# Kernel tuning notes

Measured on AMD Instinct MI355X. Metric: run time of the kernel, lower is better.

The kernel has to match this reference:

```python
import jax, jax.numpy as jnp
import numpy as np

B, L, E = 4, 2048, 1024
H, DQ, DV = 8, 128, 128
SCALE = 1.0 / np.sqrt(DQ).astype(np.float32)


def setup_inputs() -> dict:
    key = jax.random.key(0)
    ks = jax.random.split(key, 6)
    return {
        "qInputs": jax.random.normal(ks[0], (B, L, E), dtype=jnp.float32),
        "kvInputs": jax.random.normal(ks[1], (B, L, E), dtype=jnp.float32),
        "mask": jnp.zeros((B, H, L, L), dtype=jnp.bool_),
        "W_Q": jax.random.normal(ks[2], (E, H * DQ), dtype=jnp.float32) * 0.02,
        "W_K": jax.random.normal(ks[3], (E, H * DQ), dtype=jnp.float32) * 0.02,
        "W_V": jax.random.normal(ks[4], (E, H * DV), dtype=jnp.float32) * 0.02,
        "W_fc": jax.random.normal(ks[5], (H * DV, E), dtype=jnp.float32) * 0.02,
    }


def reference(qInputs, kvInputs, mask, W_Q, W_K, W_V, W_fc):
    b, lq, _ = qInputs.shape
    lk = kvInputs.shape[1]
    # Projections -> [B, H, L, D]
    Q = (qInputs @ W_Q).reshape(b, lq, H, DQ).transpose(0, 2, 1, 3)
    K = (kvInputs @ W_K).reshape(b, lk, H, DQ).transpose(0, 2, 1, 3)
    V = (kvInputs @ W_V).reshape(b, lk, H, DV).transpose(0, 2, 1, 3)
    # Scaled dot-product with additive mask fill of -1e9
    scores = jnp.einsum("bhqd,bhkd->bhqk", Q, K) * SCALE
    scores = jnp.where(mask, jnp.float32(-1e9), scores)
    attn = jax.nn.softmax(scores, axis=-1)
    ctx = jnp.einsum("bhqk,bhkd->bhqd", attn, V)
    ctx = ctx.transpose(0, 2, 1, 3).reshape(b, lq, H * DV)
    return ctx @ W_fc
```

## Files before the change

kernel.cpp:

```cpp
#include <hip/hip_runtime.h>
#include <stdint.h>

#define LQ 2048
#define EDIM 1024
#define HN 8
#define DH 128
#define BATCH 4
#define SCALE_LOG2E 0.12753785051263942f

typedef short bf16x8 __attribute__((ext_vector_type(8)));
typedef float f32x4 __attribute__((ext_vector_type(4)));
typedef unsigned short u16;
typedef unsigned short u16x4 __attribute__((ext_vector_type(4)));

__device__ __forceinline__ u16 f2bf(float f) {
  union { float f; uint32_t u; } c; c.f = f;
  uint32_t u = c.u;
  return (u16)((u + 0x7fffu + ((u >> 16) & 1u)) >> 16);
}

__device__ __forceinline__ void async16(const void* g, void* l) {
  __builtin_amdgcn_global_load_lds((const __attribute__((address_space(1))) void*)g,
                                   (__attribute__((address_space(3))) void*)l, 16, 0, 0);
}

__device__ __forceinline__ uint32_t lds_b(const u16* p) {
  return (uint32_t)(uintptr_t)(__attribute__((address_space(3))) const u16*)p;
}
__device__ __forceinline__ void ldsr4_issue(bf16x8& d0, bf16x8& d1, bf16x8& d2, bf16x8& d3,
                                            uint32_t a0, uint32_t a1, uint32_t a2, uint32_t a3) {
  asm volatile("ds_read_b128 %0, %4\n\t"
               "ds_read_b128 %1, %5\n\t"
               "ds_read_b128 %2, %6\n\t"
               "ds_read_b128 %3, %7"
               : "=&v"(d0), "=&v"(d1), "=&v"(d2), "=&v"(d3)
               : "v"(a0), "v"(a1), "v"(a2), "v"(a3));
}
template <int N>
__device__ __forceinline__ void lgkm_wait_sb() {
  asm volatile("s_waitcnt lgkmcnt(%0)" :: "n"(N) : "memory");
  __builtin_amdgcn_sched_barrier(0);
}
__device__ __forceinline__ uint32_t cvtpk(float lo, float hi) {
  uint32_t r;
  asm("v_cvt_pk_bf16_f32 %0, %1, %2" : "=v"(r) : "v"(lo), "v"(hi));
  return r;
}
__device__ __forceinline__ void plane_swap(uint32_t& a, uint32_t& b) {
#if __has_builtin(__builtin_amdgcn_permlane32_swap) && __has_builtin(__builtin_amdgcn_permlane16_swap)
  auto r1 = __builtin_amdgcn_permlane32_swap(a, b, false, false);
  auto r2 = __builtin_amdgcn_permlane16_swap(r1[0], r1[1], false, false);
  a = r2[0];
  b = r2[1];
#else
  asm("s_nop 1\n\t"
      "v_permlane32_swap_b32 %0, %1\n\t"
      "s_nop 1\n\t"
      "v_permlane16_swap_b32 %0, %1\n\t"
      "s_nop 1"
      : "+v"(a), "+v"(b));
#endif
}
__device__ __forceinline__ float xorsum16(float x) {
#if __has_builtin(__builtin_amdgcn_permlane16_swap)
  union { float f; uint32_t u; } c; c.f = x;
  auto r = __builtin_amdgcn_permlane16_swap(c.u, c.u, false, false);
  union { uint32_t u; float f; } a, b; a.u = r[0]; b.u = r[1];
  return a.f + b.f;
#else
  return x + __shfl_xor(x, 16);
#endif
}
__device__ __forceinline__ float xorsum32(float x) {
#if __has_builtin(__builtin_amdgcn_permlane32_swap)
  union { float f; uint32_t u; } c; c.f = x;
  auto r = __builtin_amdgcn_permlane32_swap(c.u, c.u, false, false);
  union { uint32_t u; float f; } a, b; a.u = r[0]; b.u = r[1];
  return a.f + b.f;
#else
  return x + __shfl_xor(x, 32);
#endif
}
__device__ __forceinline__ void swz64(int& x, int& y) {
  const int f = x + 64 * y;
  x = (f & 7) * 8 + ((f >> 3) & 7);
  y = f >> 6;
}

__global__ __launch_bounds__(256) void prep_kernel(const float* __restrict__ qIn, const float* __restrict__ kvIn,
                                                   const float* __restrict__ w0, const float* __restrict__ w1,
                                                   const float* __restrict__ w2, const float* __restrict__ w3,
                                                   u16* __restrict__ oq, u16* __restrict__ okv,
                                                   u16* __restrict__ o0, u16* __restrict__ o1,
                                                   u16* __restrict__ o2, u16* __restrict__ o3) {
  __shared__ float tile[32][33];
  const int bid = blockIdx.x;
  const int t = threadIdx.x;
  if (bid < 16384) {
    const float* in = (bid >= 8192) ? kvIn : qIn;
    u16* out = (bid >= 8192) ? okv : oq;
    size_t i = (size_t)(bid & 8191) * 256 + t;
    float4 v = ((const float4*)in)[i];
    u16x4 o;
    o.x = f2bf(v.x); o.y = f2bf(v.y); o.z = f2bf(v.z); o.w = f2bf(v.w);
    ((u16x4*)out)[i] = o;
  } else {
    const int idx = bid - 16384;
    const int z = idx >> 10;
    const int rem = idx & 1023;
    const float* in; u16* out;
    switch (z) {
      case 0: in = w0; out = o0; break;
      case 1: in = w1; out = o1; break;
      case 2: in = w2; out = o2; break;
      default: in = w3; out = o3; break;
    }
    const int tx = t & 31, ty = t >> 5;
    const int x0 = (rem & 31) * 32;
    const int y0 = (rem >> 5) * 32;
#pragma unroll
    for (int j = 0; j < 32; j += 8)
      tile[ty + j][tx] = in[(size_t)(y0 + ty + j) * EDIM + x0 + tx];
    __syncthreads();
#pragma unroll
    for (int j = 0; j < 32; j += 8)
      out[(size_t)(x0 + ty + j) * EDIM + (y0 + tx)] = f2bf(tile[tx][ty + j]);
  }
}

struct GemmCore {
  template <typename EpiF>
  static __device__ __forceinline__ void run(const u16* __restrict__ A, const u16* __restrict__ Bt,
                                             int m0, int n0, u16* As, u16* Bs, EpiF epi) {
    const int tid = threadIdx.x;
    const int l = tid & 63;
    const int w = tid >> 6;
    const int wm = (w >> 1) * 64;
    const int wn = (w & 1) * 64;
    const int fm = l & 15;
    const int q4 = l >> 4;
    const int f7 = fm & 7;
    f32x4 acc[4][4] = {};
    for (int k0 = 0; k0 < EDIM; k0 += 64) {
      __syncthreads();
#pragma unroll
      for (int ii = 0; ii < 4; ++ii) {
        const int rloc = w * 32 + ii * 8 + (l >> 3);
        const int cs = (l & 7) ^ (rloc & 7);
        async16(A + (size_t)(m0 + rloc) * EDIM + k0 + cs * 8, &As[(w * 32 + ii * 8) * 64 + l * 8]);
        async16(Bt + (size_t)(n0 + rloc) * EDIM + k0 + cs * 8, &Bs[(w * 32 + ii * 8) * 64 + l * 8]);
      }
      __syncthreads();
#pragma unroll
      for (int ks = 0; ks < 2; ++ks) {
        const int coff = ((ks * 4 + q4) ^ f7) * 8;
        bf16x8 a[4], b[4];
#pragma unroll
        for (int i = 0; i < 4; ++i) a[i] = *(const bf16x8*)&As[(wm + i * 16 + fm) * 64 + coff];
#pragma unroll
        for (int j = 0; j < 4; ++j) b[j] = *(const bf16x8*)&Bs[(wn + j * 16 + fm) * 64 + coff];
#pragma unroll
        for (int i = 0; i < 4; ++i)
#pragma unroll
          for (int j = 0; j < 4; ++j)
            acc[i][j] = __builtin_amdgcn_mfma_f32_16x16x32_bf16(a[i], b[j], acc[i][j], 0, 0, 0);
      }
    }
    const int rr = q4 * 4;
#pragma unroll
    for (int i = 0; i < 4; ++i)
#pragma unroll
      for (int j = 0; j < 4; ++j)
#pragma unroll
        for (int r = 0; r < 4; ++r)
          epi(m0 + wm + i * 16 + rr + r, n0 + wn + j * 16 + fm, acc[i][j][r]);
  }
};

__global__ __launch_bounds__(256) void qkv_gemm(const u16* __restrict__ xq, const u16* __restrict__ xkv,
                                                const u16* __restrict__ WqT, const u16* __restrict__ WkT,
                                                const u16* __restrict__ WvT,
                                                u16* __restrict__ Qb, u16* __restrict__ Kb,
                                                u16* __restrict__ Vt) {
  __shared__ __align__(16) u16 As[128 * 64];
  __shared__ __align__(16) u16 Bs[128 * 64];
  const int z = blockIdx.z;
  int bx = blockIdx.x, by = blockIdx.y;
  swz64(bx, by);
  if (z == 0) {
    GemmCore::run(xq, WqT, bx * 128, by * 128, As, Bs,
                  [&](int gm, int gn, float v) { Qb[(size_t)gm * EDIM + gn] = f2bf(v * SCALE_LOG2E); });
  } else if (z == 1) {
    GemmCore::run(xkv, WkT, bx * 128, by * 128, As, Bs,
                  [&](int gm, int gn, float v) { Kb[(size_t)gm * EDIM + gn] = f2bf(v); });
  } else {
    GemmCore::run(WvT, xkv, by * 128, bx * 128, As, Bs,
                  [&](int gm, int gn, float v) {
                    Vt[((size_t)(gn >> 11) * 1024 + gm) * 2048 + (gn & 2047)] = f2bf(v);
                  });
  }
}

__global__ __launch_bounds__(256) void out_gemm(const u16* __restrict__ ctx, const u16* __restrict__ WfcT,
                                                float* __restrict__ out) {
  __shared__ __align__(16) u16 As[128 * 64];
  __shared__ __align__(16) u16 Bs[128 * 64];
  int bx = blockIdx.x, by = blockIdx.y;
  swz64(bx, by);
  GemmCore::run(ctx, WfcT, bx * 128, by * 128, As, Bs,
                [&](int gm, int gn, float v) { out[(size_t)gm * EDIM + gn] = v; });
}

__global__ __launch_bounds__(256, 2) void attn_kernel(const u16* __restrict__ Qb, const u16* __restrict__ Kb,
                                                      const u16* __restrict__ Vt,
                                                      const unsigned char* __restrict__ mask,
                                                      u16* __restrict__ ctx) {
  __shared__ __align__(16) u16 Ktile[2][64 * 128];
  __shared__ __align__(16) u16 Vtile[2][128 * 64];
  const int tid = threadIdx.x;
  const int l = tid & 63;
  const int w = tid >> 6;
  const int flat = blockIdx.x;
  const int xcd = flat & 7;
  const int idx = flat >> 3;
  const int panel = xcd * 4 + (idx >> 4);
  const int qt = idx & 15;
  const int h = panel & 7;
  const int b = panel >> 3;
  const int fm = l & 15;
  const int q4 = l >> 4;
  const int fk = q4 * 8;
  const int f7 = fm & 7;
  const int qbase = qt * 128 + w * 32;
  const int bh = b * HN + h;

  const u16* Kbh = Kb + (size_t)b * LQ * EDIM + h * DH;
  const u16* Vth = Vt + (size_t)bh * DH * LQ;
  const size_t mbase = (size_t)bh * (size_t)LQ * LQ;
  const unsigned char* mscan = mask + mbase + (size_t)(qbase + (l >> 1)) * LQ + (l & 1) * 64;

  bf16x8 qf[2][4];
#pragma unroll
  for (int mt = 0; mt < 2; ++mt)
#pragma unroll
    for (int ks = 0; ks < 4; ++ks)
      qf[mt][ks] = *(const bf16x8*)(Qb + (size_t)(b * LQ + qbase + mt * 16 + fm) * EDIM + h * DH + ks * 32 + fk);

  uint32_t curAcc = 0, nxtAcc = 0;
#pragma unroll
  for (int j = 0; j < 4; ++j) {
    uint4 mv = *(const uint4*)(mscan + j * 16);
    curAcc |= mv.x | mv.y | mv.z | mv.w;
  }

  auto stageK = [&](int kt_, int buf) {
#pragma unroll
    for (int ii = 0; ii < 4; ++ii) {
      const int i = w * 4 + ii;
      const int row = i * 4 + (l >> 4);
      const int g = (l & 15) ^ (row & 7);
      async16(Kbh + (size_t)(kt_ * 64 + row) * EDIM + g * 8, &Ktile[buf][i * 512 + l * 8]);
    }
  };
  auto stageV = [&](int kt_, int buf) {
#pragma unroll
    for (int ii = 0; ii < 4; ++ii) {
      const int i = w * 4 + ii;
      const int row = i * 8 + (l >> 3);
      const int g = (l & 7) ^ (row & 7);
      async16(Vth + (size_t)row * LQ + kt_ * 64 + g * 8, &Vtile[buf][i * 512 + l * 8]);
    }
  };

  stageK(0, 0);
  stageV(0, 0);

  f32x4 o[2][8] = {};
  float lsumv[2] = {0.f, 0.f};

  for (int it = 0; it < 32; ++it) {
    const int cur = it & 1;
    __syncthreads();
    if (it + 1 < 32) { stageK(it + 1, 1 - cur); stageV(it + 1, 1 - cur); }

    if ((it & 1) == 0) {
      if (it > 0) curAcc = nxtAcc;
      nxtAcc = 0;
      const int tn = (it >> 1) + 1;
      if (tn < 16) {
        const unsigned char* ms = mscan + tn * 128;
#pragma unroll
        for (int j = 0; j < 4; ++j) {
          uint4 mv = *(const uint4*)(ms + j * 16);
          nxtAcc |= mv.x | mv.y | mv.z | mv.w;
        }
      }
    }
    const int hasMask = __any(curAcc != 0);

    const u16* KT = &Ktile[cur][0];
    const u16* VT = &Vtile[cur][0];

    f32x4 st[4][2] = {};
    bf16x8 kf[2][4];
    bf16x8 v0, v1, v2, v3, v4, v5, v6, v7;
    bf16x8 x0, x1, x2, x3, x4, x5, x6, x7;
    {
      const int slot = q4 ^ f7;
      ldsr4_issue(kf[0][0], kf[0][1], kf[0][2], kf[0][3],
                  lds_b(KT + (0 * 16 + fm) * 128 + slot * 8),
                  lds_b(KT + (1 * 16 + fm) * 128 + slot * 8),
                  lds_b(KT + (2 * 16 + fm) * 128 + slot * 8),
                  lds_b(KT + (3 * 16 + fm) * 128 + slot * 8));
    }
#pragma unroll
    for (int ks = 0; ks < 3; ++ks) {
      const int c = ks & 1;
      const int slot = ((ks + 1) * 4 + q4) ^ f7;
      ldsr4_issue(kf[c ^ 1][0], kf[c ^ 1][1], kf[c ^ 1][2], kf[c ^ 1][3],
                  lds_b(KT + (0 * 16 + fm) * 128 + slot * 8),
                  lds_b(KT + (1 * 16 + fm) * 128 + slot * 8),
                  lds_b(KT + (2 * 16 + fm) * 128 + slot * 8),
                  lds_b(KT + (3 * 16 + fm) * 128 + slot * 8));
      lgkm_wait_sb<4>();
      __builtin_amdgcn_s_setprio(1);
#pragma unroll
      for (int mt = 0; mt < 2; ++mt) {
        st[0][mt] = __builtin_amdgcn_mfma_f32_16x16x32_bf16(kf[c][0], qf[mt][ks], st[0][mt], 0, 0, 0);
        st[1][mt] = __builtin_amdgcn_mfma_f32_16x16x32_bf16(kf[c][1], qf[mt][ks], st[1][mt], 0, 0, 0);
        st[2][mt] = __builtin_amdgcn_mfma_f32_16x16x32_bf16(kf[c][2], qf[mt][ks], st[2][mt], 0, 0, 0);
        st[3][mt] = __builtin_amdgcn_mfma_f32_16x16x32_bf16(kf[c][3], qf[mt][ks], st[3][mt], 0, 0, 0);
      }
      __builtin_amdgcn_s_setprio(0);
    }
    {
      const int vs0 = q4 ^ f7;
      ldsr4_issue(v0, v1, v2, v3,
                  lds_b(VT + (0 * 16 + fm) * 64 + vs0 * 8), lds_b(VT + (1 * 16 + fm) * 64 + vs0 * 8),
                  lds_b(VT + (2 * 16 + fm) * 64 + vs0 * 8), lds_b(VT + (3 * 16 + fm) * 64 + vs0 * 8));
      ldsr4_issue(v4, v5, v6, v7,
                  lds_b(VT + (4 * 16 + fm) * 64 + vs0 * 8), lds_b(VT + (5 * 16 + fm) * 64 + vs0 * 8),
                  lds_b(VT + (6 * 16 + fm) * 64 + vs0 * 8), lds_b(VT + (7 * 16 + fm) * 64 + vs0 * 8));
      lgkm_wait_sb<8>();
      __builtin_amdgcn_s_setprio(1);
#pragma unroll
      for (int mt = 0; mt < 2; ++mt) {
        st[0][mt] = __builtin_amdgcn_mfma_f32_16x16x32_bf16(kf[1][0], qf[mt][3], st[0][mt], 0, 0, 0);
        st[1][mt] = __builtin_amdgcn_mfma_f32_16x16x32_bf16(kf[1][1], qf[mt][3], st[1][mt], 0, 0, 0);
        st[2][mt] = __builtin_amdgcn_mfma_f32_16x16x32_bf16(kf[1][2], qf[mt][3], st[2][mt], 0, 0, 0);
        st[3][mt] = __builtin_amdgcn_mfma_f32_16x16x32_bf16(kf[1][3], qf[mt][3], st[3][mt], 0, 0, 0);
      }
      __builtin_amdgcn_s_setprio(0);
    }

    uint32_t pk[2][4][2];
    float sA[2], sB[2];
    bf16x8 paf0, paf1;
#pragma unroll
    for (int mt = 0; mt < 2; ++mt) {
      float sum = 0.f;
      if (hasMask) {
        const unsigned char* mrow = mask + mbase + (size_t)(qbase + mt * 16 + fm) * LQ + it * 64 + q4 * 4;
#pragma unroll
        for (int kt = 0; kt < 2; ++kt) {
          const uint32_t mv = *(const uint32_t*)(mrow + kt * 16);
#pragma unroll
          for (int r = 0; r < 4; ++r) {
            float e = ((mv >> (8 * r)) & 0xffu) ? 0.f : exp2f(st[kt][mt][r]);
            st[kt][mt][r] = e;
            sum += e;
          }
        }
      } else {
#pragma unroll
        for (int kt = 0; kt < 2; ++kt)
#pragma unroll
          for (int r = 0; r < 4; ++r) {
            float e = exp2f(st[kt][mt][r]);
            st[kt][mt][r] = e;
            sum += e;
          }
      }
      sA[mt] = sum;
      pk[mt][0][0] = cvtpk(st[0][mt][0], st[0][mt][1]);
      pk[mt][0][1] = cvtpk(st[0][mt][2], st[0][mt][3]);
      pk[mt][1][0] = cvtpk(st[1][mt][0], st[1][mt][1]);
      pk[mt][1][1] = cvtpk(st[1][mt][2], st[1][mt][3]);
    }
    {
      union { uint32_t u[4]; bf16x8 v; } fb;
      uint32_t e0 = pk[0][0][0], f0 = pk[0][1][0];
      uint32_t e1 = pk[0][0][1], f1 = pk[0][1][1];
      plane_swap(e0, f0); plane_swap(e1, f1);
      fb.u[0] = e0; fb.u[1] = e1; fb.u[2] = f0; fb.u[3] = f1;
      paf0 = fb.v;
      uint32_t g0 = pk[1][0][0], h0 = pk[1][1][0];
      uint32_t g1 = pk[1][0][1], h1 = pk[1][1][1];
      plane_swap(g0, h0); plane_swap(g1, h1);
      fb.u[0] = g0; fb.u[1] = g1; fb.u[2] = h0; fb.u[3] = h1;
      paf1 = fb.v;
    }
    {
      const int vs1 = (4 + q4) ^ f7;
      ldsr4_issue(x0, x1, x2, x3,
                  lds_b(VT + (0 * 16 + fm) * 64 + vs1 * 8), lds_b(VT + (1 * 16 + fm) * 64 + vs1 * 8),
                  lds_b(VT + (2 * 16 + fm) * 64 + vs1 * 8), lds_b(VT + (3 * 16 + fm) * 64 + vs1 * 8));
      ldsr4_issue(x4, x5, x6, x7,
                  lds_b(VT + (4 * 16 + fm) * 64 + vs1 * 8), lds_b(VT + (5 * 16 + fm) * 64 + vs1 * 8),
                  lds_b(VT + (6 * 16 + fm) * 64 + vs1 * 8), lds_b(VT + (7 * 16 + fm) * 64 + vs1 * 8));
    }
    lgkm_wait_sb<8>();
    __builtin_amdgcn_s_setprio(1);
    o[0][0] = __builtin_amdgcn_mfma_f32_16x16x32_bf16(paf0, v0, o[0][0], 0, 0, 0);
    o[1][0] = __builtin_amdgcn_mfma_f32_16x16x32_bf16(paf1, v0, o[1][0], 0, 0, 0);
    o[0][1] = __builtin_amdgcn_mfma_f32_16x16x32_bf16(paf0, v1, o[0][1], 0, 0, 0);
    o[1][1] = __builtin_amdgcn_mfma_f32_16x16x32_bf16(paf1, v1, o[1][1], 0, 0, 0);
    o[0][2] = __builtin_amdgcn_mfma_f32_16x16x32_bf16(paf0, v2, o[0][2], 0, 0, 0);
    o[1][2] = __builtin_amdgcn_mfma_f32_16x16x32_bf16(paf1, v2, o[1][2], 0, 0, 0);
    o[0][3] = __builtin_amdgcn_mfma_f32_16x16x32_bf16(paf0, v3, o[0][3], 0, 0, 0);
    o[1][3] = __builtin_amdgcn_mfma_f32_16x16x32_bf16(paf1, v3, o[1][3], 0, 0, 0);
    o[0][4] = __builtin_amdgcn_mfma_f32_16x16x32_bf16(paf0, v4, o[0][4], 0, 0, 0);
    o[1][4] = __builtin_amdgcn_mfma_f32_16x16x32_bf16(paf1, v4, o[1][4], 0, 0, 0);
    o[0][5] = __builtin_amdgcn_mfma_f32_16x16x32_bf16(paf0, v5, o[0][5], 0, 0, 0);
    o[1][5] = __builtin_amdgcn_mfma_f32_16x16x32_bf16(paf1, v5, o[1][5], 0, 0, 0);
    o[0][6] = __builtin_amdgcn_mfma_f32_16x16x32_bf16(paf0, v6, o[0][6], 0, 0, 0);
    o[1][6] = __builtin_amdgcn_mfma_f32_16x16x32_bf16(paf1, v6, o[1][6], 0, 0, 0);
    o[0][7] = __builtin_amdgcn_mfma_f32_16x16x32_bf16(paf0, v7, o[0][7], 0, 0, 0);
    o[1][7] = __builtin_amdgcn_mfma_f32_16x16x32_bf16(paf1, v7, o[1][7], 0, 0, 0);
    __builtin_amdgcn_s_setprio(0);

#pragma unroll
    for (int mt = 0; mt < 2; ++mt) {
      float sum = 0.f;
      if (hasMask) {
        const unsigned char* mrow = mask + mbase + (size_t)(qbase + mt * 16 + fm) * LQ + it * 64 + q4 * 4;
#pragma unroll
        for (int kt = 2; kt < 4; ++kt) {
          const uint32_t mv = *(const uint32_t*)(mrow + kt * 16);
#pragma unroll
          for (int r = 0; r < 4; ++r) {
            float e = ((mv >> (8 * r)) & 0xffu) ? 0.f : exp2f(st[kt][mt][r]);
            st[kt][mt][r] = e;
            sum += e;
          }
        }
      } else {
#pragma unroll
        for (int kt = 2; kt < 4; ++kt)
#pragma unroll
          for (int r = 0; r < 4; ++r) {
            float e = exp2f(st[kt][mt][r]);
            st[kt][mt][r] = e;
            sum += e;
          }
      }
      sB[mt] = sum;
      pk[mt][2][0] = cvtpk(st[2][mt][0], st[2][mt][1]);
      pk[mt][2][1] = cvtpk(st[2][mt][2], st[2][mt][3]);
      pk[mt][3][0] = cvtpk(st[3][mt][0], st[3][mt][1]);
      pk[mt][3][1] = cvtpk(st[3][mt][2], st[3][mt][3]);
    }
    {
      union { uint32_t u[4]; bf16x8 v; } fb;
      uint32_t e0 = pk[0][2][0], f0 = pk[0][3][0];
      uint32_t e1 = pk[0][2][1], f1 = pk[0][3][1];
      plane_swap(e0, f0); plane_swap(e1, f1);
      fb.u[0] = e0; fb.u[1] = e1; fb.u[2] = f0; fb.u[3] = f1;
      paf0 = fb.v;
      uint32_t g0 = pk[1][2][0], h0 = pk[1][3][0];
      uint32_t g1 = pk[1][2][1], h1 = pk[1][3][1];
      plane_swap(g0, h0); plane_swap(g1, h1);
      fb.u[0] = g0; fb.u[1] = g1; fb.u[2] = h0; fb.u[3] = h1;
      paf1 = fb.v;
    }
#pragma unroll
    for (int mt = 0; mt < 2; ++mt) {
      float t = sA[mt] + sB[mt];
      lsumv[mt] += xorsum32(xorsum16(t));
    }

    lgkm_wait_sb<0>();
    __builtin_amdgcn_s_setprio(1);
    o[0][0] = __builtin_amdgcn_mfma_f32_16x16x32_bf16(paf0, x0, o[0][0], 0, 0, 0);
    o[1][0] = __builtin_amdgcn_mfma_f32_16x16x32_bf16(paf1, x0, o[1][0], 0, 0, 0);
    o[0][1] = __builtin_amdgcn_mfma_f32_16x16x32_bf16(paf0, x1, o[0][1], 0, 0, 0);
    o[1][1] = __builtin_amdgcn_mfma_f32_16x16x32_bf16(paf1, x1, o[1][1], 0, 0, 0);
    o[0][2] = __builtin_amdgcn_mfma_f32_16x16x32_bf16(paf0, x2, o[0][2], 0, 0, 0);
    o[1][2] = __builtin_amdgcn_mfma_f32_16x16x32_bf16(paf1, x2, o[1][2], 0, 0, 0);
    o[0][3] = __builtin_amdgcn_mfma_f32_16x16x32_bf16(paf0, x3, o[0][3], 0, 0, 0);
    o[1][3] = __builtin_amdgcn_mfma_f32_16x16x32_bf16(paf1, x3, o[1][3], 0, 0, 0);
    o[0][4] = __builtin_amdgcn_mfma_f32_16x16x32_bf16(paf0, x4, o[0][4], 0, 0, 0);
    o[1][4] = __builtin_amdgcn_mfma_f32_16x16x32_bf16(paf1, x4, o[1][4], 0, 0, 0);
    o[0][5] = __builtin_amdgcn_mfma_f32_16x16x32_bf16(paf0, x5, o[0][5], 0, 0, 0);
    o[1][5] = __builtin_amdgcn_mfma_f32_16x16x32_bf16(paf1, x5, o[1][5], 0, 0, 0);
    o[0][6] = __builtin_amdgcn_mfma_f32_16x16x32_bf16(paf0, x6, o[0][6], 0, 0, 0);
    o[1][6] = __builtin_amdgcn_mfma_f32_16x16x32_bf16(paf1, x6, o[1][6], 0, 0, 0);
    o[0][7] = __builtin_amdgcn_mfma_f32_16x16x32_bf16(paf0, x7, o[0][7], 0, 0, 0);
    o[1][7] = __builtin_amdgcn_mfma_f32_16x16x32_bf16(paf1, x7, o[1][7], 0, 0, 0);
    __builtin_amdgcn_s_setprio(0);
  }

#pragma unroll
  for (int mt = 0; mt < 2; ++mt)
#pragma unroll
    for (int r = 0; r < 4; ++r) {
      float inv = 1.f / __shfl(lsumv[mt], q4 * 4 + r);
      int gq = b * LQ + qbase + mt * 16 + q4 * 4 + r;
#pragma unroll
      for (int dt = 0; dt < 8; ++dt)
        ctx[(size_t)gq * EDIM + h * DH + dt * 16 + fm] = f2bf(o[mt][dt][r] * inv);
    }
}

extern "C" void kernel_launch(void* const* d_in, const int* in_sizes, int n_in,
                              void* d_out, int out_size, void* d_ws, size_t ws_size,
                              hipStream_t stream) {
  const float* qIn = (const float*)d_in[0];
  const float* kvIn = (const float*)d_in[1];
  const unsigned char* mask = (const unsigned char*)d_in[2];
  const float* W_Q = (const float*)d_in[3];
  const float* W_K = (const float*)d_in[4];
  const float* W_V = (const float*)d_in[5];
  const float* W_fc = (const float*)d_in[6];
  float* out = (float*)d_out;

  uint8_t* ws = (uint8_t*)d_ws;
  const size_t MB = 1u << 20;
  u16* xq   = (u16*)(ws);
  u16* xkv  = (u16*)(ws + 16 * MB);
  u16* WqT  = (u16*)(ws + 32 * MB);
  u16* WkT  = (u16*)(ws + 34 * MB);
  u16* WvT  = (u16*)(ws + 36 * MB);
  u16* WfcT = (u16*)(ws + 38 * MB);
  u16* Qb   = (u16*)(ws + 40 * MB);
  u16* Kb   = (u16*)(ws + 56 * MB);
  u16* Vt   = (u16*)(ws + 72 * MB);
  u16* ctx  = (u16*)(ws + 88 * MB);

  prep_kernel<<<20480, 256, 0, stream>>>(qIn, kvIn, W_Q, W_K, W_V, W_fc,
                                         xq, xkv, WqT, WkT, WvT, WfcT);
  qkv_gemm<<<dim3(64, 8, 3), 256, 0, stream>>>(xq, xkv, WqT, WkT, WvT, Qb, Kb, Vt);
  attn_kernel<<<512, 256, 0, stream>>>(Qb, Kb, Vt, mask, ctx);
  out_gemm<<<dim3(64, 8), 256, 0, stream>>>(ctx, WfcT, out);
}
```

Baseline: 812.6 us.

## Double per-wave query rows in attention to reuse K/V tiles across 64 queries

```diff
diff --git a/kernel.cpp b/kernel.cpp
--- a/kernel.cpp
+++ b/kernel.cpp
@@ -211,7 +211,7 @@
                 [&](int gm, int gn, float v) { out[(size_t)gm * EDIM + gn] = v; });
 }
 
-__global__ __launch_bounds__(256, 2) void attn_kernel(const u16* __restrict__ Qb, const u16* __restrict__ Kb,
+__global__ __launch_bounds__(256, 1) void attn_kernel(const u16* __restrict__ Qb, const u16* __restrict__ Kb,
                                                       const u16* __restrict__ Vt,
                                                       const unsigned char* __restrict__ mask,
                                                       u16* __restrict__ ctx) {
@@ -223,32 +223,32 @@
   const int flat = blockIdx.x;
   const int xcd = flat & 7;
   const int idx = flat >> 3;
-  const int panel = xcd * 4 + (idx >> 4);
-  const int qt = idx & 15;
+  const int panel = xcd * 4 + (idx >> 3);
+  const int qt = idx & 7;
   const int h = panel & 7;
   const int b = panel >> 3;
   const int fm = l & 15;
   const int q4 = l >> 4;
   const int fk = q4 * 8;
   const int f7 = fm & 7;
-  const int qbase = qt * 128 + w * 32;
+  const int qbase = qt * 256 + w * 64;
   const int bh = b * HN + h;
 
   const u16* Kbh = Kb + (size_t)b * LQ * EDIM + h * DH;
   const u16* Vth = Vt + (size_t)bh * DH * LQ;
   const size_t mbase = (size_t)bh * (size_t)LQ * LQ;
-  const unsigned char* mscan = mask + mbase + (size_t)(qbase + (l >> 1)) * LQ + (l & 1) * 64;
-
-  bf16x8 qf[2][4];
-#pragma unroll
-  for (int mt = 0; mt < 2; ++mt)
+  const unsigned char* mscan = mask + mbase + (size_t)(qbase + l) * LQ;
+
+  bf16x8 qf[4][4];
+#pragma unroll
+  for (int mt = 0; mt < 4; ++mt)
 #pragma unroll
     for (int ks = 0; ks < 4; ++ks)
       qf[mt][ks] = *(const bf16x8*)(Qb + (size_t)(b * LQ + qbase + mt * 16 + fm) * EDIM + h * DH + ks * 32 + fk);
 
   uint32_t curAcc = 0, nxtAcc = 0;
 #pragma unroll
-  for (int j = 0; j < 4; ++j) {
+  for (int j = 0; j < 8; ++j) {
     uint4 mv = *(const uint4*)(mscan + j * 16);
     curAcc |= mv.x | mv.y | mv.z | mv.w;
   }
@@ -275,8 +275,8 @@
   stageK(0, 0);
   stageV(0, 0);
 
-  f32x4 o[2][8] = {};
-  float lsumv[2] = {0.f, 0.f};
+  f32x4 o[4][8] = {};
+  float lsumv[4] = {0.f, 0.f, 0.f, 0.f};
 
   for (int it = 0; it < 32; ++it) {
     const int cur = it & 1;
@@ -290,7 +290,7 @@
       if (tn < 16) {
         const unsigned char* ms = mscan + tn * 128;
 #pragma unroll
-        for (int j = 0; j < 4; ++j) {
+        for (int j = 0; j < 8; ++j) {
           uint4 mv = *(const uint4*)(ms + j * 16);
           nxtAcc |= mv.x | mv.y | mv.z | mv.w;
         }
@@ -301,10 +301,10 @@
     const u16* KT = &Ktile[cur][0];
     const u16* VT = &Vtile[cur][0];
 
-    f32x4 st[4][2] = {};
+    f32x4 st[4][4] = {};
     bf16x8 kf[2][4];
-    bf16x8 v0, v1, v2, v3, v4, v5, v6, v7;
-    bf16x8 x0, x1, x2, x3, x4, x5, x6, x7;
+    bf16x8 vv[8];
+    bf16x8 xx[8];
     {
       const int slot = q4 ^ f7;
       ldsr4_issue(kf[0][0], kf[0][1], kf[0][2], kf[0][3],
@@ -325,7 +325,7 @@
       lgkm_wait_sb<4>();
       __builtin_amdgcn_s_setprio(1);
 #pragma unroll
-      for (int mt = 0; mt < 2; ++mt) {
+      for (int mt = 0; mt < 4; ++mt) {
         st[0][mt] = __builtin_amdgcn_mfma_f32_16x16x32_bf16(kf[c][0], qf[mt][ks], st[0][mt], 0, 0, 0);
         st[1][mt] = __builtin_amdgcn_mfma_f32_16x16x32_bf16(kf[c][1], qf[mt][ks], st[1][mt], 0, 0, 0);
         st[2][mt] = __builtin_amdgcn_mfma_f32_16x16x32_bf16(kf[c][2], qf[mt][ks], st[2][mt], 0, 0, 0);
@@ -335,16 +335,16 @@
     }
     {
       const int vs0 = q4 ^ f7;
-      ldsr4_issue(v0, v1, v2, v3,
+      ldsr4_issue(vv[0], vv[1], vv[2], vv[3],
                   lds_b(VT + (0 * 16 + fm) * 64 + vs0 * 8), lds_b(VT + (1 * 16 + fm) * 64 + vs0 * 8),
                   lds_b(VT + (2 * 16 + fm) * 64 + vs0 * 8), lds_b(VT + (3 * 16 + fm) * 64 + vs0 * 8));
-      ldsr4_issue(v4, v5, v6, v7,
+      ldsr4_issue(vv[4], vv[5], vv[6], vv[7],
                   lds_b(VT + (4 * 16 + fm) * 64 + vs0 * 8), lds_b(VT + (5 * 16 + fm) * 64 + vs0 * 8),
                   lds_b(VT + (6 * 16 + fm) * 64 + vs0 * 8), lds_b(VT + (7 * 16 + fm) * 64 + vs0 * 8));
       lgkm_wait_sb<8>();
       __builtin_amdgcn_s_setprio(1);
 #pragma unroll
-      for (int mt = 0; mt < 2; ++mt) {
+      for (int mt = 0; mt < 4; ++mt) {
         st[0][mt] = __builtin_amdgcn_mfma_f32_16x16x32_bf16(kf[1][0], qf[mt][3], st[0][mt], 0, 0, 0);
         st[1][mt] = __builtin_amdgcn_mfma_f32_16x16x32_bf16(kf[1][1], qf[mt][3], st[1][mt], 0, 0, 0);
         st[2][mt] = __builtin_amdgcn_mfma_f32_16x16x32_bf16(kf[1][2], qf[mt][3], st[2][mt], 0, 0, 0);
@@ -353,11 +353,11 @@
       __builtin_amdgcn_s_setprio(0);
     }
 
-    uint32_t pk[2][4][2];
-    float sA[2], sB[2];
-    bf16x8 paf0, paf1;
-#pragma unroll
-    for (int mt = 0; mt < 2; ++mt) {
+    uint32_t pk[4][4][2];
+    float sA[4], sB[4];
+    bf16x8 paf[4];
+#pragma unroll
+    for (int mt = 0; mt < 4; ++mt) {
       float sum = 0.f;
       if (hasMask) {
         const unsigned char* mrow = mask + mbase + (size_t)(qbase + mt * 16 + fm) * LQ + it * 64 + q4 * 4;
@@ -387,50 +387,35 @@
       pk[mt][1][0] = cvtpk(st[1][mt][0], st[1][mt][1]);
       pk[mt][1][1] = cvtpk(st[1][mt][2], st[1][mt][3]);
     }
-    {
+#pragma unroll
+    for (int mt = 0; mt < 4; ++mt) {
       union { uint32_t u[4]; bf16x8 v; } fb;
-      uint32_t e0 = pk[0][0][0], f0 = pk[0][1][0];
-      uint32_t e1 = pk[0][0][1], f1 = pk[0][1][1];
+      uint32_t e0 = pk[mt][0][0], f0 = pk[mt][1][0];
+      uint32_t e1 = pk[mt][0][1], f1 = pk[mt][1][1];
       plane_swap(e0, f0); plane_swap(e1, f1);
       fb.u[0] = e0; fb.u[1] = e1; fb.u[2] = f0; fb.u[3] = f1;
-      paf0 = fb.v;
-      uint32_t g0 = pk[1][0][0], h0 = pk[1][1][0];
-      uint32_t g1 = pk[1][0][1], h1 = pk[1][1][1];
-      plane_swap(g0, h0); plane_swap(g1, h1);
-      fb.u[0] = g0; fb.u[1] = g1; fb.u[2] = h0; fb.u[3] = h1;
-      paf1 = fb.v;
+      paf[mt] = fb.v;
     }
     {
       const int vs1 = (4 + q4) ^ f7;
-      ldsr4_issue(x0, x1, x2, x3,
+      ldsr4_issue(xx[0], xx[1], xx[2], xx[3],
                   lds_b(VT + (0 * 16 + fm) * 64 + vs1 * 8), lds_b(VT + (1 * 16 + fm) * 64 + vs1 * 8),
                   lds_b(VT + (2 * 16 + fm) * 64 + vs1 * 8), lds_b(VT + (3 * 16 + fm) * 64 + vs1 * 8));
-      ldsr4_issue(x4, x5, x6, x7,
+      ldsr4_issue(xx[4], xx[5], xx[6], xx[7],
                   lds_b(VT + (4 * 16 + fm) * 64 + vs1 * 8), lds_b(VT + (5 * 16 + fm) * 64 + vs1 * 8),
                   lds_b(VT + (6 * 16 + fm) * 64 + vs1 * 8), lds_b(VT + (7 * 16 + fm) * 64 + vs1 * 8));
     }
     lgkm_wait_sb<8>();
     __builtin_amdgcn_s_setprio(1);
-    o[0][0] = __builtin_amdgcn_mfma_f32_16x16x32_bf16(paf0, v0, o[0][0], 0, 0, 0);
-    o[1][0] = __builtin_amdgcn_mfma_f32_16x16x32_bf16(paf1, v0, o[1][0], 0, 0, 0);
-    o[0][1] = __builtin_amdgcn_mfma_f32_16x16x32_bf16(paf0, v1, o[0][1], 0, 0, 0);
-    o[1][1] = __builtin_amdgcn_mfma_f32_16x16x32_bf16(paf1, v1, o[1][1], 0, 0, 0);
-    o[0][2] = __builtin_amdgcn_mfma_f32_16x16x32_bf16(paf0, v2, o[0][2], 0, 0, 0);
-    o[1][2] = __builtin_amdgcn_mfma_f32_16x16x32_bf16(paf1, v2, o[1][2], 0, 0, 0);
-    o[0][3] = __builtin_amdgcn_mfma_f32_16x16x32_bf16(paf0, v3, o[0][3], 0, 0, 0);
-    o[1][3] = __builtin_amdgcn_mfma_f32_16x16x32_bf16(paf1, v3, o[1][3], 0, 0, 0);
-    o[0][4] = __builtin_amdgcn_mfma_f32_16x16x32_bf16(paf0, v4, o[0][4], 0, 0, 0);
-    o[1][4] = __builtin_amdgcn_mfma_f32_16x16x32_bf16(paf1, v4, o[1][4], 0, 0, 0);
-    o[0][5] = __builtin_amdgcn_mfma_f32_16x16x32_bf16(paf0, v5, o[0][5], 0, 0, 0);
-    o[1][5] = __builtin_amdgcn_mfma_f32_16x16x32_bf16(paf1, v5, o[1][5], 0, 0, 0);
-    o[0][6] = __builtin_amdgcn_mfma_f32_16x16x32_bf16(paf0, v6, o[0][6], 0, 0, 0);
-    o[1][6] = __builtin_amdgcn_mfma_f32_16x16x32_bf16(paf1, v6, o[1][6], 0, 0, 0);
-    o[0][7] = __builtin_amdgcn_mfma_f32_16x16x32_bf16(paf0, v7, o[0][7], 0, 0, 0);
-    o[1][7] = __builtin_amdgcn_mfma_f32_16x16x32_bf16(paf1, v7, o[1][7], 0, 0, 0);
+#pragma unroll
+    for (int dt = 0; dt < 8; ++dt)
+#pragma unroll
+      for (int mt = 0; mt < 4; ++mt)
+        o[mt][dt] = __builtin_amdgcn_mfma_f32_16x16x32_bf16(paf[mt], vv[dt], o[mt][dt], 0, 0, 0);
     __builtin_amdgcn_s_setprio(0);
 
 #pragma unroll
-    for (int mt = 0; mt < 2; ++mt) {
+    for (int mt = 0; mt < 4; ++mt) {
       float sum = 0.f;
       if (hasMask) {
         const unsigned char* mrow = mask + mbase + (size_t)(qbase + mt * 16 + fm) * LQ + it * 64 + q4 * 4;
@@ -460,48 +445,33 @@
       pk[mt][3][0] = cvtpk(st[3][mt][0], st[3][mt][1]);
       pk[mt][3][1] = cvtpk(st[3][mt][2], st[3][mt][3]);
     }
-    {
+#pragma unroll
+    for (int mt = 0; mt < 4; ++mt) {
       union { uint32_t u[4]; bf16x8 v; } fb;
-      uint32_t e0 = pk[0][2][0], f0 = pk[0][3][0];
-      uint32_t e1 = pk[0][2][1], f1 = pk[0][3][1];
+      uint32_t e0 = pk[mt][2][0], f0 = pk[mt][3][0];
+      uint32_t e1 = pk[mt][2][1], f1 = pk[mt][3][1];
       plane_swap(e0, f0); plane_swap(e1, f1);
       fb.u[0] = e0; fb.u[1] = e1; fb.u[2] = f0; fb.u[3] = f1;
-      paf0 = fb.v;
-      uint32_t g0 = pk[1][2][0], h0 = pk[1][3][0];
-      uint32_t g1 = pk[1][2][1], h1 = pk[1][3][1];
-      plane_swap(g0, h0); plane_swap(g1, h1);
-      fb.u[0] = g0; fb.u[1] = g1; fb.u[2] = h0; fb.u[3] = h1;
-      paf1 = fb.v;
-    }
-#pragma unroll
-    for (int mt = 0; mt < 2; ++mt) {
+      paf[mt] = fb.v;
+    }
+#pragma unroll
+    for (int mt = 0; mt < 4; ++mt) {
       float t = sA[mt] + sB[mt];
       lsumv[mt] += xorsum32(xorsum16(t));
     }
 
     lgkm_wait_sb<0>();
     __builtin_amdgcn_s_setprio(1);
-    o[0][0] = __builtin_amdgcn_mfma_f32_16x16x32_bf16(paf0, x0, o[0][0], 0, 0, 0);
-    o[1][0] = __builtin_amdgcn_mfma_f32_16x16x32_bf16(paf1, x0, o[1][0], 0, 0, 0);
-    o[0][1] = __builtin_amdgcn_mfma_f32_16x16x32_bf16(paf0, x1, o[0][1], 0, 0, 0);
-    o[1][1] = __builtin_amdgcn_mfma_f32_16x16x32_bf16(paf1, x1, o[1][1], 0, 0, 0);
-    o[0][2] = __builtin_amdgcn_mfma_f32_16x16x32_bf16(paf0, x2, o[0][2], 0, 0, 0);
-    o[1][2] = __builtin_amdgcn_mfma_f32_16x16x32_bf16(paf1, x2, o[1][2], 0, 0, 0);
-    o[0][3] = __builtin_amdgcn_mfma_f32_16x16x32_bf16(paf0, x3, o[0][3], 0, 0, 0);
-    o[1][3] = __builtin_amdgcn_mfma_f32_16x16x32_bf16(paf1, x3, o[1][3], 0, 0, 0);
-    o[0][4] = __builtin_amdgcn_mfma_f32_16x16x32_bf16(paf0, x4, o[0][4], 0, 0, 0);
-    o[1][4] = __builtin_amdgcn_mfma_f32_16x16x32_bf16(paf1, x4, o[1][4], 0, 0, 0);
-    o[0][5] = __builtin_amdgcn_mfma_f32_16x16x32_bf16(paf0, x5, o[0][5], 0, 0, 0);
-    o[1][5] = __builtin_amdgcn_mfma_f32_16x16x32_bf16(paf1, x5, o[1][5], 0, 0, 0);
-    o[0][6] = __builtin_amdgcn_mfma_f32_16x16x32_bf16(paf0, x6, o[0][6], 0, 0, 0);
-    o[1][6] = __builtin_amdgcn_mfma_f32_16x16x32_bf16(paf1, x6, o[1][6], 0, 0, 0);
-    o[0][7] = __builtin_amdgcn_mfma_f32_16x16x32_bf16(paf0, x7, o[0][7], 0, 0, 0);
-    o[1][7] = __builtin_amdgcn_mfma_f32_16x16x32_bf16(paf1, x7, o[1][7], 0, 0, 0);
+#pragma unroll
+    for (int dt = 0; dt < 8; ++dt)
+#pragma unroll
+      for (int mt = 0; mt < 4; ++mt)
+        o[mt][dt] = __builtin_amdgcn_mfma_f32_16x16x32_bf16(paf[mt], xx[dt], o[mt][dt], 0, 0, 0);
     __builtin_amdgcn_s_setprio(0);
   }
 
 #pragma unroll
-  for (int mt = 0; mt < 2; ++mt)
+  for (int mt = 0; mt < 4; ++mt)
 #pragma unroll
     for (int r = 0; r < 4; ++r) {
       float inv = 1.f / __shfl(lsumv[mt], q4 * 4 + r);
@@ -540,6 +510,6 @@
   prep_kernel<<<20480, 256, 0, stream>>>(qIn, kvIn, W_Q, W_K, W_V, W_fc,
                                          xq, xkv, WqT, WkT, WvT, WfcT);
   qkv_gemm<<<dim3(64, 8, 3), 256, 0, stream>>>(xq, xkv, WqT, WkT, WvT, Qb, Kb, Vt);
-  attn_kernel<<<512, 256, 0, stream>>>(Qb, Kb, Vt, mask, ctx);
+  attn_kernel<<<256, 256, 0, stream>>>(Qb, Kb, Vt, mask, ctx);
   out_gemm<<<dim3(64, 8), 256, 0, stream>>>(ctx, WfcT, out);
 }
```

Result: no change. 828.5 us (+2.0%).
